# Kernel optimization log

Hardware: AMD Instinct MI355X
Metric: run time of the kernel (lower is better)

The kernel has to match this reference:

```python
import jax, jax.numpy as jnp
import numpy as np

N = 16384      # instances (cells) per bag
IN = 2000      # input_dim (genes)
E1, E2 = 1024, 512   # encoder_dims
HID = 512      # hidden_dim
NH, HD = 8, 64 # num_heads, head_dim
LK = 256       # linformer_k
EPROJ_N = 10000  # fixed in-dim of E/F projections
NEXP, MH = 4, 256  # moe experts, moe hidden (= classifier_dims[0])
C1, C2, NC = 256, 128, 2


def _ln(x, g, b):
    m = jnp.mean(x, axis=-1, keepdims=True)
    v = jnp.var(x, axis=-1, keepdims=True)
    return (x - m) * jax.lax.rsqrt(v + 1e-5) * g + b


def setup_inputs() -> dict:
    key = jax.random.key(0)
    ks = jax.random.split(key, 24)
    s = 0.02
    f32 = jnp.float32
    inp = {
        'x': jax.random.normal(ks[0], (N, IN), dtype=f32),
        'enc_w1': jax.random.normal(ks[1], (IN, E1), dtype=f32) * s,
        'enc_b1': jnp.zeros((E1,), f32),
        'enc_w2': jax.random.normal(ks[2], (E1, E2), dtype=f32) * s,
        'enc_b2': jnp.zeros((E2,), f32),
        'enc_w3': jax.random.normal(ks[3], (E2, HID), dtype=f32) * s,
        'enc_b3': jnp.zeros((HID,), f32),
        'q_w': jax.random.normal(ks[4], (HID, HID), dtype=f32) * s,
        'q_b': jnp.zeros((HID,), f32),
        'k_w': jax.random.normal(ks[5], (HID, HID), dtype=f32) * s,
        'k_b': jnp.zeros((HID,), f32),
        'v_w': jax.random.normal(ks[6], (HID, HID), dtype=f32) * s,
        'v_b': jnp.zeros((HID,), f32),
        'o_w': jax.random.normal(ks[7], (HID, HID), dtype=f32) * s,
        'o_b': jnp.zeros((HID,), f32),
        'E_w': jax.random.normal(ks[8], (LK, EPROJ_N), dtype=f32) * s,  # nn.Linear(10000, k).weight
        'F_w': jax.random.normal(ks[9], (LK, EPROJ_N), dtype=f32) * s,
        'ln1_g': jnp.ones((HID,), f32), 'ln1_b': jnp.zeros((HID,), f32),
        'ln2_g': jnp.ones((HID,), f32), 'ln2_b': jnp.zeros((HID,), f32),
        'gate_w': jax.random.normal(ks[10], (HID, NEXP), dtype=f32) * s,
        'gate_b': jnp.zeros((NEXP,), f32),
        'moe_w1': jax.random.normal(ks[11], (NEXP, HID, MH), dtype=f32) * s,
        'moe_b1': jnp.zeros((NEXP, MH), f32),
        'moe_w2': jax.random.normal(ks[12], (NEXP, MH), dtype=f32) * s,
        'moe_b2': jnp.zeros((NEXP,), f32),
        'cls_w1': jax.random.normal(ks[13], (HID, C1), dtype=f32) * s,
        'cls_b1': jnp.zeros((C1,), f32),
        'cls_w2': jax.random.normal(ks[14], (C1, C2), dtype=f32) * s,
        'cls_b2': jnp.zeros((C2,), f32),
        'cls_w3': jax.random.normal(ks[15], (C2, NC), dtype=f32) * s,
        'cls_b3': jnp.zeros((NC,), f32),
    }
    return inp


def reference(x, enc_w1, enc_b1, enc_w2, enc_b2, enc_w3, enc_b3,
              q_w, q_b, k_w, k_b, v_w, v_b, o_w, o_b, E_w, F_w,
              ln1_g, ln1_b, ln2_g, ln2_b,
              gate_w, gate_b, moe_w1, moe_b1, moe_w2, moe_b2,
              cls_w1, cls_b1, cls_w2, cls_b2, cls_w3, cls_b3):
    # --- instance encoder (chunking in torch is math-equivalent to one pass) ---
    h = jax.nn.relu(x @ enc_w1 + enc_b1)
    h = jax.nn.relu(h @ enc_w2 + enc_b2)
    feat = jax.nn.relu(h @ enc_w3 + enc_b3)          # [N, HID]
    # dropouts / InstanceDropout are identity at inference

    # --- linformer attention (single bag, batch of 1) ---
    Q = (feat @ q_w + q_b).reshape(N, NH, HD).transpose(1, 0, 2)  # [H, N, D]
    K = (feat @ k_w + k_b).reshape(N, NH, HD).transpose(1, 0, 2)
    V = (feat @ v_w + v_b).reshape(N, NH, HD).transpose(1, 0, 2)
    # N > linformer_k and the torch inner check (seq_len <= weight.size(0)=LK)
    # is false, so E/F are bilinearly resized from [10000, LK] to [LK, N], then
    # transposed to [N, LK] (matches F.interpolate align_corners=False).
    E_m = jax.image.resize(E_w.T, (LK, N), method='bilinear').T   # [N, LK]
    F_m = jax.image.resize(F_w.T, (LK, N), method='bilinear').T   # [N, LK]
    Kc = jnp.einsum('hnd,nk->hkd', K, E_m)           # [H, LK, D]
    Vc = jnp.einsum('hnd,nk->hkd', V, F_m)           # [H, LK, D]
    scores = jax.nn.softmax(jnp.einsum('hnd,hkd->hnk', Q, Kc) * (HD ** -0.5), axis=-1)
    ao = jnp.einsum('hnk,hkd->hnd', scores, Vc)      # [H, N, D]
    attn_out = ao.transpose(1, 0, 2).reshape(N, HID) @ o_w + o_b

    att = _ln(attn_out + feat, ln1_g, ln1_b)
    att = _ln(att, ln2_g, ln2_b)                     # [N, HID]

    # --- MoE MIL aggregation: gated mixture of per-expert attention pooling ---
    gates = jax.nn.softmax(jnp.mean(att, axis=0) @ gate_w + gate_b)       # [E]
    Hm = jnp.tanh(jnp.einsum('nd,edh->enh', att, moe_w1) + moe_b1[:, None, :])
    sc = jnp.einsum('enh,eh->en', Hm, moe_w2) + moe_b2[:, None]           # [E, N]
    a = jax.nn.softmax(sc, axis=1)                   # per-expert instance attention
    attn_weights = gates @ a                         # [N]
    bag = attn_weights @ att                         # [HID]

    # --- classifier ---
    c = jax.nn.relu(bag @ cls_w1 + cls_b1)
    c = jax.nn.relu(c @ cls_w2 + cls_b2)
    disease = c @ cls_w3 + cls_b3                    # [NC]
    # use_domain_adaptation=False -> no domain output
    return (bag, disease, attn_weights)
```

## Files before the change

kernel.cpp:

```cpp
#include <hip/hip_runtime.h>

#define DI __device__ __forceinline__

DI float bf2f(unsigned short u){ unsigned int v = ((unsigned int)u)<<16; float f; __builtin_memcpy(&f,&v,4); return f; }
DI unsigned short f2bf(float f){ unsigned int v; __builtin_memcpy(&v,&f,4); v = v + 0x7FFFu + ((v>>16)&1u); return (unsigned short)(v>>16); }

typedef __attribute__((ext_vector_type(8))) short bf16x8;
typedef __attribute__((ext_vector_type(4))) short short4v;
typedef __attribute__((ext_vector_type(4))) float f32x4;

#define GLD_LDS16(src, dst) __builtin_amdgcn_global_load_lds( \
    (const __attribute__((address_space(1))) void*)(src), \
    (__attribute__((address_space(3))) void*)(dst), 16, 0, 0)

DI void barrier_() { asm volatile("" ::: "memory"); __builtin_amdgcn_s_barrier(); asm volatile("" ::: "memory"); }

template<int ACT>
__global__ __launch_bounds__(256,2) void gemm5_k(
    const unsigned short* __restrict__ A, const unsigned short* __restrict__ Bt,
    const float* __restrict__ bias, unsigned short* __restrict__ C,
    int K, int lda, int ldb, int ldc)
{
  __shared__ unsigned short As[2][8192];
  __shared__ unsigned short Bs[2][8192];
  const int tid = threadIdx.x, lane = tid & 63, wid = tid >> 6;
  const int wm = wid >> 1, wn = wid & 1;
  const int q = lane >> 4, r15 = lane & 15;
  const int nx = gridDim.x;
  const int bid = blockIdx.x + nx*blockIdx.y;
  const int cpx = (nx*gridDim.y) >> 3;
  const int wg = (bid & 7)*cpx + (bid >> 3);
  const long long mBase = (long long)(wg / nx) << 7;
  const long long nBase = (long long)(wg % nx) << 7;

  f32x4 acc[4][4];
#pragma unroll
  for (int i=0;i<4;i++)
#pragma unroll
    for (int j=0;j<4;j++)
#pragma unroll
      for (int r=0;r<4;r++) acc[i][j][r] = 0.f;

  const int NT = K >> 6;

#define G5_STA(j, nb, kk) { const int d_ = tid + ((j)<<8); const int row_ = d_>>3, c_ = d_&7, sc_ = c_ ^ (row_&7); \
    GLD_LDS16(A + (mBase+row_)*(long long)lda + (kk) + (sc_<<3), &As[nb][d_<<3]); }
#define G5_STB(j, nb, kk) { const int d_ = tid + ((j)<<8); const int row_ = d_>>3, c_ = d_&7, sc_ = c_ ^ (row_&7); \
    GLD_LDS16(Bt + (nBase+row_)*(long long)ldb + (kk) + (sc_<<3), &Bs[nb][d_<<3]); }

  G5_STB(0,0,0); G5_STB(2,0,0); G5_STB(1,0,0); G5_STB(3,0,0);
  G5_STA(0,0,0); G5_STA(2,0,0); G5_STA(1,0,0); G5_STA(3,0,0);

  for (int t=0; t<NT; ++t) {
    const int b = t & 1, nb = b ^ 1;
    const bool more = (t+1 < NT);
    const int k1 = (t+1) << 6;
    bf16x8 aL[4], aH[4], bL[4], bH[4];

    asm volatile("s_waitcnt vmcnt(2)" ::: "memory");
    barrier_();
#pragma unroll
    for (int mi=0; mi<2; ++mi)
#pragma unroll
      for (int ks=0; ks<2; ++ks) {
        const int row = (wm<<6) + (mi<<4) + r15;
        const int ch = ((ks<<2)+q) ^ (row&7);
        aL[mi*2+ks] = *(const bf16x8*)&As[b][(row<<6) + (ch<<3)];
      }
#pragma unroll
    for (int ni=0; ni<2; ++ni)
#pragma unroll
      for (int ks=0; ks<2; ++ks) {
        const int col = (wn<<6) + (ni<<4) + r15;
        const int ch = ((ks<<2)+q) ^ (col&7);
        bL[ni*2+ks] = *(const bf16x8*)&Bs[b][(col<<6) + (ch<<3)];
      }
    if (more) { G5_STB(0,nb,k1); G5_STB(2,nb,k1); }
    __builtin_amdgcn_s_setprio(1);
#pragma unroll
    for (int mi=0; mi<2; ++mi)
#pragma unroll
      for (int ni=0; ni<2; ++ni)
#pragma unroll
        for (int ks=0; ks<2; ++ks)
          acc[mi][ni] = __builtin_amdgcn_mfma_f32_16x16x32_bf16(aL[mi*2+ks], bL[ni*2+ks], acc[mi][ni], 0,0,0);
    __builtin_amdgcn_s_setprio(0);
    barrier_();

#pragma unroll
    for (int ni=0; ni<2; ++ni)
#pragma unroll
      for (int ks=0; ks<2; ++ks) {
        const int col = (wn<<6) + ((ni+2)<<4) + r15;
        const int ch = ((ks<<2)+q) ^ (col&7);
        bH[ni*2+ks] = *(const bf16x8*)&Bs[b][(col<<6) + (ch<<3)];
      }
    if (more) { G5_STB(1,nb,k1); G5_STB(3,nb,k1); }
    __builtin_amdgcn_s_setprio(1);
#pragma unroll
    for (int mi=0; mi<2; ++mi)
#pragma unroll
      for (int ni=0; ni<2; ++ni)
#pragma unroll
        for (int ks=0; ks<2; ++ks)
          acc[mi][ni+2] = __builtin_amdgcn_mfma_f32_16x16x32_bf16(aL[mi*2+ks], bH[ni*2+ks], acc[mi][ni+2], 0,0,0);
    __builtin_amdgcn_s_setprio(0);

    if (more) { asm volatile("s_waitcnt vmcnt(4)" ::: "memory"); }
    else      { asm volatile("s_waitcnt vmcnt(0)" ::: "memory"); }
    barrier_();
#pragma unroll
    for (int mi=0; mi<2; ++mi)
#pragma unroll
      for (int ks=0; ks<2; ++ks) {
        const int row = (wm<<6) + ((mi+2)<<4) + r15;
        const int ch = ((ks<<2)+q) ^ (row&7);
        aH[mi*2+ks] = *(const bf16x8*)&As[b][(row<<6) + (ch<<3)];
      }
    if (more) { G5_STA(0,nb,k1); G5_STA(2,nb,k1); }
    __builtin_amdgcn_s_setprio(1);
#pragma unroll
    for (int mi=0; mi<2; ++mi)
#pragma unroll
      for (int ni=0; ni<2; ++ni)
#pragma unroll
        for (int ks=0; ks<2; ++ks)
          acc[mi+2][ni] = __builtin_amdgcn_mfma_f32_16x16x32_bf16(aH[mi*2+ks], bL[ni*2+ks], acc[mi+2][ni], 0,0,0);
    __builtin_amdgcn_s_setprio(0);
    barrier_();

    if (more) { G5_STA(1,nb,k1); G5_STA(3,nb,k1); }
    __builtin_amdgcn_s_setprio(1);
#pragma unroll
    for (int mi=0; mi<2; ++mi)
#pragma unroll
      for (int ni=0; ni<2; ++ni)
#pragma unroll
        for (int ks=0; ks<2; ++ks)
          acc[mi+2][ni+2] = __builtin_amdgcn_mfma_f32_16x16x32_bf16(aH[mi*2+ks], bH[ni*2+ks], acc[mi+2][ni+2], 0,0,0);
    __builtin_amdgcn_s_setprio(0);
  }
#undef G5_STA
#undef G5_STB

#pragma unroll
  for (int ni=0; ni<4; ++ni) {
    const long long n = nBase + (wn<<6) + (ni<<4) + r15;
    const float bval = bias[n];
#pragma unroll
    for (int mi=0; mi<4; ++mi) {
#pragma unroll
      for (int r=0; r<4; ++r) {
        const long long m = mBase + (wm<<6) + (mi<<4) + (q<<2) + r;
        float v = acc[mi][ni][r] + bval;
        if constexpr (ACT==1) v = fmaxf(v, 0.f);
        C[m*(long long)ldc + n] = f2bf(v);
      }
    }
  }
}

template<int ACT, bool MOE>
__global__ __launch_bounds__(512,2) void gemm4_k(
    const unsigned short* __restrict__ A, const unsigned short* __restrict__ Bt,
    const float* __restrict__ bias, unsigned short* __restrict__ C,
    const float* __restrict__ w2, float* __restrict__ scp,
    int K, int lda, int ldb, int ldc)
{
  __shared__ unsigned short As[2][16384];
  __shared__ unsigned short Bs[2][16384];
  const int tid = threadIdx.x, lane = tid & 63, wid = tid >> 6;
  const int wm = wid >> 2, wn = wid & 3;
  const int q = lane >> 4, r15 = lane & 15;
  const int nx = gridDim.x;
  const int bid = blockIdx.x + nx*blockIdx.y;
  const int cpx = (nx*gridDim.y) >> 3;
  const int wg = (bid & 7)*cpx + (bid >> 3);
  const long long mBase = (long long)(wg / nx) << 8;
  const long long nBase = (long long)(wg % nx) << 8;

  f32x4 acc[8][4];
#pragma unroll
  for (int i=0;i<8;i++)
#pragma unroll
    for (int j=0;j<4;j++)
#pragma unroll
      for (int r=0;r<4;r++) acc[i][j][r] = 0.f;

  const int NT = K >> 6;

#define G4_STA(j, nb, kk) { const int d_ = tid + ((j)<<9); const int row_ = d_>>3, c_ = d_&7, sc_ = c_ ^ (row_&7); \
    GLD_LDS16(A + (mBase+row_)*(long long)lda + (kk) + (sc_<<3), &As[nb][d_<<3]); }
#define G4_STB(j, nb, kk) { const int d_ = tid + ((j)<<9); const int row_ = d_>>3, c_ = d_&7, sc_ = c_ ^ (row_&7); \
    GLD_LDS16(Bt + (nBase+row_)*(long long)ldb + (kk) + (sc_<<3), &Bs[nb][d_<<3]); }

  G4_STB(0,0,0); G4_STB(1,0,0); G4_STB(2,0,0); G4_STB(3,0,0);
  G4_STA(0,0,0); G4_STA(2,0,0); G4_STA(1,0,0); G4_STA(3,0,0);

  for (int t=0; t<NT; ++t) {
    const int b = t & 1, nb = b ^ 1;
    const bool more = (t+1 < NT);
    const int k1 = (t+1) << 6;
    bf16x8 aF[8], bL[4], bH[4];

    asm volatile("s_waitcnt vmcnt(2)" ::: "memory");
    barrier_();
#pragma unroll
    for (int mi=0; mi<4; ++mi)
#pragma unroll
      for (int ks=0; ks<2; ++ks) {
        const int row = (wm<<7) + (mi<<4) + r15;
        const int ch = ((ks<<2)+q) ^ (row&7);
        aF[mi*2+ks] = *(const bf16x8*)&As[b][(row<<6) + (ch<<3)];
      }
#pragma unroll
    for (int ni=0; ni<2; ++ni)
#pragma unroll
      for (int ks=0; ks<2; ++ks) {
        const int col = (wn<<6) + (ni<<4) + r15;
        const int ch = ((ks<<2)+q) ^ (col&7);
        bL[ni*2+ks] = *(const bf16x8*)&Bs[b][(col<<6) + (ch<<3)];
      }
    if (more) { G4_STB(0,nb,k1); G4_STB(1,nb,k1); }
    __builtin_amdgcn_s_setprio(1);
#pragma unroll
    for (int mi=0; mi<4; ++mi)
#pragma unroll
      for (int ni=0; ni<2; ++ni)
#pragma unroll
        for (int ks=0; ks<2; ++ks)
          acc[mi][ni] = __builtin_amdgcn_mfma_f32_16x16x32_bf16(aF[mi*2+ks], bL[ni*2+ks], acc[mi][ni], 0,0,0);
    __builtin_amdgcn_s_setprio(0);
    barrier_();

#pragma unroll
    for (int ni=0; ni<2; ++ni)
#pragma unroll
      for (int ks=0; ks<2; ++ks) {
        const int col = (wn<<6) + ((ni+2)<<4) + r15;
        const int ch = ((ks<<2)+q) ^ (col&7);
        bH[ni*2+ks] = *(const bf16x8*)&Bs[b][(col<<6) + (ch<<3)];
      }
    if (more) { G4_STB(2,nb,k1); G4_STB(3,nb,k1); }
    __builtin_amdgcn_s_setprio(1);
#pragma unroll
    for (int mi=0; mi<4; ++mi)
#pragma unroll
      for (int ni=0; ni<2; ++ni)
#pragma unroll
        for (int ks=0; ks<2; ++ks)
          acc[mi][ni+2] = __builtin_amdgcn_mfma_f32_16x16x32_bf16(aF[mi*2+ks], bH[ni*2+ks], acc[mi][ni+2], 0,0,0);
    __builtin_amdgcn_s_setprio(0);

    if (more) { asm volatile("s_waitcnt vmcnt(4)" ::: "memory"); }
    else      { asm volatile("s_waitcnt vmcnt(0)" ::: "memory"); }
    barrier_();
#pragma unroll
    for (int mi=0; mi<4; ++mi)
#pragma unroll
      for (int ks=0; ks<2; ++ks) {
        const int row = (wm<<7) + ((mi+4)<<4) + r15;
        const int ch = ((ks<<2)+q) ^ (row&7);
        aF[mi*2+ks] = *(const bf16x8*)&As[b][(row<<6) + (ch<<3)];
      }
    if (more) { G4_STA(0,nb,k1); G4_STA(2,nb,k1); }
    __builtin_amdgcn_s_setprio(1);
#pragma unroll
    for (int mi=0; mi<4; ++mi)
#pragma unroll
      for (int ni=0; ni<2; ++ni)
#pragma unroll
        for (int ks=0; ks<2; ++ks)
          acc[mi+4][ni] = __builtin_amdgcn_mfma_f32_16x16x32_bf16(aF[mi*2+ks], bL[ni*2+ks], acc[mi+4][ni], 0,0,0);
    __builtin_amdgcn_s_setprio(0);
    barrier_();

    if (more) { G4_STA(1,nb,k1); G4_STA(3,nb,k1); }
    __builtin_amdgcn_s_setprio(1);
#pragma unroll
    for (int mi=0; mi<4; ++mi)
#pragma unroll
      for (int ni=0; ni<2; ++ni)
#pragma unroll
        for (int ks=0; ks<2; ++ks)
          acc[mi+4][ni+2] = __builtin_amdgcn_mfma_f32_16x16x32_bf16(aF[mi*2+ks], bH[ni*2+ks], acc[mi+4][ni+2], 0,0,0);
    __builtin_amdgcn_s_setprio(0);
  }
#undef G4_STA
#undef G4_STB

  if constexpr (MOE) {
    const int e = (int)(nBase >> 8);
#pragma unroll
    for (int mi=0; mi<8; ++mi) {
#pragma unroll
      for (int r=0; r<4; ++r) {
        float p = 0.f;
#pragma unroll
        for (int ni=0; ni<4; ++ni) {
          const int n = (int)nBase + (wn<<6) + (ni<<4) + r15;
          const float v = acc[mi][ni][r] + bias[n];
          const float th = 1.f - 2.f/(__expf(2.f*v) + 1.f);
          p += th * w2[n];
        }
        p += __shfl_xor(p,1,64); p += __shfl_xor(p,2,64);
        p += __shfl_xor(p,4,64); p += __shfl_xor(p,8,64);
        if (r15 == 0) {
          const long long m = mBase + (wm<<7) + (mi<<4) + (q<<2) + r;
          atomicAdd(scp + ((long long)e<<14) + m, p);
        }
      }
    }
  } else {
#pragma unroll
    for (int ni=0; ni<4; ++ni) {
      const long long n = nBase + (wn<<6) + (ni<<4) + r15;
      const float bval = bias[n];
#pragma unroll
      for (int mi=0; mi<8; ++mi) {
#pragma unroll
        for (int r=0; r<4; ++r) {
          const long long m = mBase + (wm<<7) + (mi<<4) + (q<<2) + r;
          float v = acc[mi][ni][r] + bval;
          if constexpr (ACT==1) v = fmaxf(v, 0.f);
          C[m*(long long)ldc + n] = f2bf(v);
        }
      }
    }
  }
}

DI void transpose64(const float* __restrict__ src, unsigned short* __restrict__ dst,
                    int K, int N, int Kpad, int k0, int n0, float (*tile)[65], int tid)
{
  const int c = tid & 63, rg = tid >> 6;
#pragma unroll
  for (int j=0;j<16;j++){
    const int r = (j<<2) + rg;
    const int k = k0 + r;
    tile[r][c] = (k < K) ? src[(long long)k*N + n0 + c] : 0.f;
  }
  __syncthreads();
#pragma unroll
  for (int j=0;j<16;j++){
    const int nn = (j<<2) + rg;
    dst[(long long)(n0+nn)*Kpad + k0 + c] = f2bf(tile[c][nn]);
  }
}

__global__ __launch_bounds__(256) void prep_k(
    const float* __restrict__ x, unsigned short* __restrict__ xb,
    const float* __restrict__ enc_w1, unsigned short* __restrict__ w1t,
    const float* __restrict__ enc_w2, unsigned short* __restrict__ w2t,
    const float* __restrict__ enc_w3, const float* __restrict__ q_w,
    const float* __restrict__ k_w, const float* __restrict__ v_w, const float* __restrict__ o_w,
    unsigned short* __restrict__ w3t, unsigned short* __restrict__ qkvw, unsigned short* __restrict__ owt,
    const float* __restrict__ moe_w1, unsigned short* __restrict__ mwt,
    const float* __restrict__ Ew, const float* __restrict__ Fw, float* __restrict__ t1,
    const float* __restrict__ qb, const float* __restrict__ kb, const float* __restrict__ vb,
    float* __restrict__ qkvb)
{
  __shared__ float tile[64][65];
  const int b = blockIdx.x, tid = threadIdx.x;
  if (b < 512) {
    const int k = b & 255, which = b >> 8, c = tid;
    const float* Wr = (which ? Fw : Ew) + (long long)c*10000;
    const float ksc = 39.0625f, inv = 1.f/39.0625f;
    const float sf = (k + 0.5f)*ksc - 0.5f;
    int ilo = (int)ceilf(sf - ksc); if (ilo < 0) ilo = 0;
    int ihi = (int)floorf(sf + ksc); if (ihi > 9999) ihi = 9999;
    float acc = 0.f, wsum = 0.f;
    int i = ilo;
    for (; i + 8 <= ihi + 1; i += 8) {
      float v[8];
#pragma unroll
      for (int j=0;j<8;j++) v[j] = Wr[i+j];
#pragma unroll
      for (int j=0;j<8;j++){
        const float w = fmaxf(1.f - fabsf(sf - (float)(i+j))*inv, 0.f);
        acc += w*v[j]; wsum += w;
      }
    }
    for (; i <= ihi; ++i) {
      const float w = fmaxf(1.f - fabsf(sf - (float)i)*inv, 0.f);
      acc += w * Wr[i]; wsum += w;
    }
    t1[(which*256 + k)*256 + c] = acc / wsum;
  } else if (b < 1024) {
    const int bb = b - 512;
    transpose64(enc_w1, w1t, 2000, 1024, 2048, (bb&31)<<6, (bb>>5)<<6, tile, tid);
  } else if (b < 1152) {
    const int bb = b - 1024;
    transpose64(enc_w2, w2t, 1024, 512, 1024, (bb&15)<<6, (bb>>4)<<6, tile, tid);
  } else if (b < 1472) {
    const int bb = b - 1152;
    const int z = bb >> 6, r = bb & 63;
    const float* s = (z==0)?enc_w3:(z==1)?q_w:(z==2)?k_w:(z==3)?v_w:o_w;
    unsigned short* d = (z==0)?w3t:(z==1)?qkvw:(z==2)?(qkvw+512*512):(z==3)?(qkvw+1024*512):owt;
    transpose64(s, d, 512, 512, 512, (r&7)<<6, (r>>3)<<6, tile, tid);
  } else if (b < 1600) {
    const int bb = b - 1472;
    const int z = bb >> 5, r = bb & 31;
    transpose64(moe_w1 + (long long)z*512*256, mwt + (long long)z*256*512,
                512, 256, 512, (r&7)<<6, (r>>3)<<6, tile, tid);
  } else if (b == 1600) {
#pragma unroll
    for (int i=0;i<6;i++){
      const int idx = i*256 + tid;
      const int wq = idx >> 9, off = idx & 511;
      const float* src = (wq==0)?qb:(wq==1)?kb:vb;
      qkvb[idx] = src[off];
    }
  } else if (b < 1985) {
    const int p = (b - 1601)*256 + tid;
    const int row = p / 6, cc = p - row*6;
    bf16x8 z8;
#pragma unroll
    for (int j=0;j<8;j++) z8[j]=0;
    *(bf16x8*)(xb + (long long)row*2048 + 2000 + cc*8) = z8;
  } else {
    const int bb = b - 1985;
    const long long base = (long long)bb*256 + tid;
#pragma unroll
    for (int j=0;j<16;j++){
      const long long id = base + (long long)j*524288;
      if (id < 8192000) {
        const float4 f = *((const float4*)x + id);
        const long long row = id / 500;
        const int col = (int)(id - row*500);
        short4v o;
        o[0]=(short)f2bf(f.x); o[1]=(short)f2bf(f.y); o[2]=(short)f2bf(f.z); o[3]=(short)f2bf(f.w);
        *(short4v*)(xb + row*2048 + (long long)col*4) = o;
      }
    }
  }
}

__global__ __launch_bounds__(512) void red_k(const unsigned short* __restrict__ qkv,
                                             float* __restrict__ red)
{
  const int c = blockIdx.x, which = blockIdx.y, j = threadIdx.x;
  const unsigned short* X = qkv + (which ? 1024 : 512);
  int nlo = 64*c - 32; if (nlo < 0) nlo = 0;
  int nhi = 64*c + 95; if (nhi > 16383) nhi = 16383;
  float acc = 0.f;
  for (int n=nlo; n<=nhi; ++n) {
    float sf = (n + 0.5f)*0.015625f - 0.5f;
    sf = fminf(fmaxf(sf, 0.f), 255.f);
    const int c0 = (int)sf;
    const float f = sf - (float)c0;
    float w = 0.f;
    if (c == c0) w = 1.f - f;
    else if (c == c0+1) w = f;
    if (w != 0.f) acc += w * bf2f(X[(long long)n*1536 + j]);
  }
  red[(which*256 + c)*512 + j] = acc;
}

__global__ __launch_bounds__(512) void kc_k(const float* __restrict__ t1, const float* __restrict__ red,
                                            unsigned short* __restrict__ Kc, unsigned short* __restrict__ Vct)
{
  const int k = blockIdx.x, which = blockIdx.y, j = threadIdx.x;
  const float* T = t1 + (which*256 + k)*256;
  const float* R = red + which*131072;
  float acc = 0.f;
  for (int c=0; c<256; ++c) acc += T[c] * R[c*512 + j];
  const int h = j >> 6, d = j & 63;
  if (which == 0) Kc [(h<<14) + (k<<6) + d] = f2bf(acc);
  else            Vct[(h<<14) + (d<<8) + k] = f2bf(acc);
}

__global__ __launch_bounds__(256) void attn_k(
    const unsigned short* __restrict__ Qg, const unsigned short* __restrict__ Kc,
    const unsigned short* __restrict__ Vct, unsigned short* __restrict__ ao)
{
  __shared__ unsigned short Ks[16384];
  __shared__ unsigned short Vs[16384];
  __shared__ unsigned short Ps[32768];
  const int h = blockIdx.y;
  const long long mBase = (long long)blockIdx.x << 7;
  const int tid = threadIdx.x, lane = tid & 63, wid = tid >> 6;
  const int q = lane >> 4, r15 = lane & 15;

#pragma unroll
  for (int it=0; it<8; ++it) {
    const int dbase = (it<<8) + (wid<<6);
    const int d = dbase + lane;
    {
      const int row = d >> 3, cc = d & 7, sc = cc ^ (row & 7);
      GLD_LDS16(Kc + (h<<14) + (row<<6) + (sc<<3), Ks + (dbase<<3));
    }
    {
      const int row = d >> 5, cc = d & 31, sc = (cc & 24) | ((cc ^ (row & 7)) & 7);
      GLD_LDS16(Vct + (h<<14) + (row<<8) + (sc<<3), Vs + (dbase<<3));
    }
  }
  __syncthreads();

  f32x4 acc[2][16];
#pragma unroll
  for (int mi=0;mi<2;mi++)
#pragma unroll
    for (int ni=0;ni<16;ni++)
#pragma unroll
      for (int r=0;r<4;r++) acc[mi][ni][r] = 0.f;

#pragma unroll
  for (int ks=0; ks<2; ++ks) {
    bf16x8 af[2];
#pragma unroll
    for (int mi=0; mi<2; ++mi) {
      const long long m = mBase + (wid<<5) + (mi<<4) + r15;
      af[mi] = *(const bf16x8*)(Qg + m*1536 + (h<<6) + (ks<<5) + (q<<3));
    }
#pragma unroll
    for (int ni=0; ni<16; ++ni) {
      const int col = (ni<<4) + r15;
      const int ch = ((ks<<2)+q) ^ (col&7);
      const bf16x8 bv = *(const bf16x8*)(Ks + (col<<6) + (ch<<3));
      acc[0][ni] = __builtin_amdgcn_mfma_f32_16x16x32_bf16(af[0], bv, acc[0][ni], 0,0,0);
      acc[1][ni] = __builtin_amdgcn_mfma_f32_16x16x32_bf16(af[1], bv, acc[1][ni], 0,0,0);
    }
  }

#pragma unroll
  for (int mi=0; mi<2; ++mi) {
#pragma unroll
    for (int r=0; r<4; ++r) {
      float mx = -3.4e38f;
#pragma unroll
      for (int ni=0; ni<16; ++ni) mx = fmaxf(mx, acc[mi][ni][r]);
      mx = fmaxf(mx, __shfl_xor(mx,1,64)); mx = fmaxf(mx, __shfl_xor(mx,2,64));
      mx = fmaxf(mx, __shfl_xor(mx,4,64)); mx = fmaxf(mx, __shfl_xor(mx,8,64));
      float s = 0.f;
#pragma unroll
      for (int ni=0; ni<16; ++ni) {
        const float e = __expf((acc[mi][ni][r] - mx)*0.125f);
        acc[mi][ni][r] = e; s += e;
      }
      s += __shfl_xor(s,1,64); s += __shfl_xor(s,2,64);
      s += __shfl_xor(s,4,64); s += __shfl_xor(s,8,64);
      const float inv = 1.f / s;
      const int row = (wid<<5) + (mi<<4) + (q<<2) + r;
#pragma unroll
      for (int ni=0; ni<16; ++ni) {
        const int col = (ni<<4) + r15;
        const int ch = col >> 3;
        const int chs = (ch & 24) | ((ch ^ (row & 7)) & 7);
        Ps[(row<<8) + (chs<<3) + (col&7)] = f2bf(acc[mi][ni][r]*inv);
      }
    }
  }
  __syncthreads();

  f32x4 o[2][4];
#pragma unroll
  for (int mi=0;mi<2;mi++)
#pragma unroll
    for (int ni=0;ni<4;ni++)
#pragma unroll
      for (int r=0;r<4;r++) o[mi][ni][r] = 0.f;

#pragma unroll
  for (int kk=0; kk<8; ++kk) {
    bf16x8 pa[2];
#pragma unroll
    for (int mi=0; mi<2; ++mi) {
      const int row = (wid<<5) + (mi<<4) + r15;
      const int ch = (kk<<2) + q;
      const int chs = (ch & 24) | ((ch ^ (row & 7)) & 7);
      pa[mi] = *(const bf16x8*)(Ps + (row<<8) + (chs<<3));
    }
#pragma unroll
    for (int ni=0; ni<4; ++ni) {
      const int vrow = (ni<<4) + r15;
      const int ch = (kk<<2) + q;
      const int chs = (ch & 24) | ((ch ^ (vrow & 7)) & 7);
      const bf16x8 bv = *(const bf16x8*)(Vs + (vrow<<8) + (chs<<3));
      o[0][ni] = __builtin_amdgcn_mfma_f32_16x16x32_bf16(pa[0], bv, o[0][ni], 0,0,0);
      o[1][ni] = __builtin_amdgcn_mfma_f32_16x16x32_bf16(pa[1], bv, o[1][ni], 0,0,0);
    }
  }
#pragma unroll
  for (int mi=0; mi<2; ++mi)
#pragma unroll
    for (int ni=0; ni<4; ++ni)
#pragma unroll
      for (int r=0; r<4; ++r) {
        const long long m = mBase + (wid<<5) + (mi<<4) + (q<<2) + r;
        ao[m*512 + (h<<6) + (ni<<4) + r15] = f2bf(o[mi][ni][r]);
      }
}

__global__ __launch_bounds__(256) void ln64_k(
    const unsigned short* __restrict__ attno, const unsigned short* __restrict__ feat,
    const float* __restrict__ g1, const float* __restrict__ b1,
    const float* __restrict__ g2, const float* __restrict__ b2,
    unsigned short* __restrict__ att, float* __restrict__ colp, float* __restrict__ scp)
{
  __shared__ float cred[4][512];
  const int tid = threadIdx.x, lane = tid & 63, wid = tid >> 6;
  const int c0 = lane << 3;
  scp[((long long)blockIdx.x<<8) + tid] = 0.f;
  float g1v[8], b1v[8], g2v[8], b2v[8];
#pragma unroll
  for (int j=0;j<8;j++){ g1v[j]=g1[c0+j]; b1v[j]=b1[c0+j]; g2v[j]=g2[c0+j]; b2v[j]=b2[c0+j]; }
  float cacc[8];
#pragma unroll
  for (int j=0;j<8;j++) cacc[j]=0.f;
  for (int rr=0; rr<16; ++rr) {
    const long long row = ((long long)blockIdx.x<<6) + (rr<<2) + wid;
    const bf16x8 a = *(const bf16x8*)(attno + (row<<9) + c0);
    const bf16x8 f = *(const bf16x8*)(feat  + (row<<9) + c0);
    float xv[8]; float s=0.f, qs=0.f;
#pragma unroll
    for (int j=0;j<8;j++){ xv[j] = bf2f((unsigned short)a[j]) + bf2f((unsigned short)f[j]); s += xv[j]; qs += xv[j]*xv[j]; }
#pragma unroll
    for (int o=32;o;o>>=1){ s += __shfl_xor(s,o,64); qs += __shfl_xor(qs,o,64); }
    float m = s*(1.f/512.f);
    float rs = rsqrtf(qs*(1.f/512.f) - m*m + 1e-5f);
    float y[8]; s=0.f; qs=0.f;
#pragma unroll
    for (int j=0;j<8;j++){ y[j] = (xv[j]-m)*rs*g1v[j] + b1v[j]; s += y[j]; qs += y[j]*y[j]; }
#pragma unroll
    for (int o=32;o;o>>=1){ s += __shfl_xor(s,o,64); qs += __shfl_xor(qs,o,64); }
    m = s*(1.f/512.f);
    rs = rsqrtf(qs*(1.f/512.f) - m*m + 1e-5f);
    bf16x8 ov;
#pragma unroll
    for (int j=0;j<8;j++){ const float z = (y[j]-m)*rs*g2v[j] + b2v[j]; cacc[j] += z; ov[j] = (short)f2bf(z); }
    *(bf16x8*)(att + (row<<9) + c0) = ov;
  }
#pragma unroll
  for (int j=0;j<8;j++) cred[wid][c0+j] = cacc[j];
  __syncthreads();
  {
    const float v0 = cred[0][tid]+cred[1][tid]+cred[2][tid]+cred[3][tid];
    const float v1 = cred[0][tid+256]+cred[1][tid+256]+cred[2][tid+256]+cred[3][tid+256];
    colp[((long long)blockIdx.x<<9)+tid]     = v0;
    colp[((long long)blockIdx.x<<9)+tid+256] = v1;
  }
}

__global__ __launch_bounds__(512) void meangates_k(const float* __restrict__ part,
    const float* __restrict__ gw, const float* __restrict__ gb, float* __restrict__ gates)
{
  __shared__ float mv[512];
  __shared__ float tmp[4];
  const int t = threadIdx.x;
  float s = 0.f;
  for (int b=0;b<256;b++) s += part[(b<<9)+t];
  mv[t] = s * (1.f/16384.f);
  __syncthreads();
  if (t < 4) {
    float a = gb[t];
    for (int d=0; d<512; ++d) a += mv[d]*gw[d*4+t];
    tmp[t] = a;
  }
  __syncthreads();
  if (t == 0) {
    const float m = fmaxf(fmaxf(tmp[0],tmp[1]),fmaxf(tmp[2],tmp[3]));
    float e[4]; float ss=0.f;
    for (int i=0;i<4;i++){ e[i]=__expf(tmp[i]-m); ss+=e[i]; }
    for (int i=0;i<4;i++) gates[i] = e[i]/ss;
  }
}

__global__ __launch_bounds__(1024) void moestat_k(const float* __restrict__ sc,
                                                  float* __restrict__ mstat, float* __restrict__ sstat)
{
  __shared__ float red[1024];
  const int e = blockIdx.x, t = threadIdx.x;
  const float* p = sc + e*16384;
  float m = -3.4e38f;
  for (int n=t; n<16384; n+=1024) m = fmaxf(m, p[n]);
  red[t] = m; __syncthreads();
  for (int o=512;o;o>>=1){ if (t<o) red[t]=fmaxf(red[t],red[t+o]); __syncthreads(); }
  m = red[0]; __syncthreads();
  float s = 0.f;
  for (int n=t; n<16384; n+=1024) s += __expf(p[n]-m);
  red[t] = s; __syncthreads();
  for (int o=512;o;o>>=1){ if (t<o) red[t]+=red[t+o]; __syncthreads(); }
  if (t==0){ mstat[e]=m; sstat[e]=red[0]; }
}

__global__ __launch_bounds__(256) void wbag_k(const unsigned short* __restrict__ att,
    const float* __restrict__ scp, const float* __restrict__ gates,
    const float* __restrict__ mstat, const float* __restrict__ sstat,
    float* __restrict__ part, float* __restrict__ dout)
{
  __shared__ float wrow[128];
  const int c = threadIdx.x;
  const long long r0 = (long long)blockIdx.x * 128;
  if (c < 128) {
    const long long n = r0 + c;
    float w = 0.f;
#pragma unroll
    for (int e=0;e<4;e++) w += gates[e]*__expf(scp[((long long)e<<14)+n]-mstat[e]) / sstat[e];
    wrow[c] = w;
    dout[514 + n] = w;
  }
  __syncthreads();
  float a0=0.f, a1=0.f;
  for (int r=0;r<128;r++){
    const float w = wrow[r];
    const unsigned short* p = att + ((r0+r)<<9);
    a0 += w*bf2f(p[c]); a1 += w*bf2f(p[c+256]);
  }
  part[((long long)blockIdx.x<<9)+c]     = a0;
  part[((long long)blockIdx.x<<9)+c+256] = a1;
}

__global__ __launch_bounds__(512) void cls2_k(const float* __restrict__ bagp,
    const float* __restrict__ w1, const float* __restrict__ b1,
    const float* __restrict__ w2, const float* __restrict__ b2,
    const float* __restrict__ w3, const float* __restrict__ b3, float* __restrict__ dout)
{
  __shared__ float bag[512]; __shared__ float c1[256]; __shared__ float c2[128];
  const int tid = threadIdx.x;
  float s = 0.f;
  for (int b=0;b<128;b++) s += bagp[(b<<9)+tid];
  bag[tid] = s; dout[tid] = s;
  __syncthreads();
  if (tid < 256) {
    float a = b1[tid];
    for (int d=0; d<512; ++d) a += bag[d]*w1[d*256+tid];
    c1[tid] = fmaxf(a, 0.f);
  }
  __syncthreads();
  if (tid < 128) {
    float a2 = b2[tid];
    for (int d=0; d<256; ++d) a2 += c1[d]*w2[d*128+tid];
    c2[tid] = fmaxf(a2, 0.f);
  }
  __syncthreads();
  if (tid < 2) {
    float a3 = b3[tid];
    for (int d=0; d<128; ++d) a3 += c2[d]*w3[d*2+tid];
    dout[512 + tid] = a3;
  }
}

extern "C" void kernel_launch(void* const* d_in, const int* in_sizes, int n_in,
                              void* d_out, int out_size, void* d_ws, size_t ws_size,
                              hipStream_t stream)
{
  (void)in_sizes; (void)n_in; (void)out_size; (void)ws_size;
  const float* x      = (const float*)d_in[0];
  const float* enc_w1 = (const float*)d_in[1];
  const float* enc_b1 = (const float*)d_in[2];
  const float* enc_w2 = (const float*)d_in[3];
  const float* enc_b2 = (const float*)d_in[4];
  const float* enc_w3 = (const float*)d_in[5];
  const float* enc_b3 = (const float*)d_in[6];
  const float* q_w    = (const float*)d_in[7];
  const float* q_b    = (const float*)d_in[8];
  const float* k_w    = (const float*)d_in[9];
  const float* k_b    = (const float*)d_in[10];
  const float* v_w    = (const float*)d_in[11];
  const float* v_b    = (const float*)d_in[12];
  const float* o_w    = (const float*)d_in[13];
  const float* o_b    = (const float*)d_in[14];
  const float* E_w    = (const float*)d_in[15];
  const float* F_w    = (const float*)d_in[16];
  const float* ln1_g  = (const float*)d_in[17];
  const float* ln1_b  = (const float*)d_in[18];
  const float* ln2_g  = (const float*)d_in[19];
  const float* ln2_b  = (const float*)d_in[20];
  const float* gate_w = (const float*)d_in[21];
  const float* gate_b = (const float*)d_in[22];
  const float* moe_w1 = (const float*)d_in[23];
  const float* moe_b1 = (const float*)d_in[24];
  const float* moe_w2 = (const float*)d_in[25];
  const float* cls_w1 = (const float*)d_in[27];
  const float* cls_b1 = (const float*)d_in[28];
  const float* cls_w2 = (const float*)d_in[29];
  const float* cls_b2 = (const float*)d_in[30];
  const float* cls_w3 = (const float*)d_in[31];
  const float* cls_b3 = (const float*)d_in[32];

  char* ws = (char*)d_ws;
  const size_t MB = 1024*1024;
  unsigned short* x_bf  = (unsigned short*)(ws + 0);
  unsigned short* h1    = (unsigned short*)(ws + 64*MB);
  unsigned short* h2    = (unsigned short*)(ws + 0);
  unsigned short* feat  = (unsigned short*)(ws + 16*MB);
  unsigned short* qkv   = (unsigned short*)(ws + 32*MB);
  unsigned short* ao    = (unsigned short*)(ws + 80*MB);
  unsigned short* attno = (unsigned short*)(ws + 0);
  unsigned short* att   = (unsigned short*)(ws + 96*MB);
  unsigned short* w1t   = (unsigned short*)(ws + 112*MB);
  unsigned short* w2t   = (unsigned short*)(ws + 116*MB);
  unsigned short* w3t   = (unsigned short*)(ws + 117*MB);
  unsigned short* qkvw  = (unsigned short*)(ws + 117*MB + 512*1024);
  unsigned short* owt   = (unsigned short*)(ws + 119*MB);
  unsigned short* mwt   = (unsigned short*)(ws + 119*MB + 512*1024);
  float*  t1b   = (float*)(ws + 120*MB + 512*1024);
  float*  redb  = (float*)(ws + 121*MB);
  unsigned short* Kcbf  = (unsigned short*)(ws + 122*MB);
  unsigned short* Vctbf = (unsigned short*)(ws + 122*MB + 256*1024);
  float*  colp  = (float*)(ws + 122*MB + 512*1024);
  float*  bagp  = (float*)(ws + 123*MB);
  float*  qkvb  = (float*)(ws + 123*MB + 256*1024);
  float*  gatesp= (float*)(ws + 123*MB + 264*1024);
  float*  scp   = (float*)(ws + 123*MB + 268*1024);
  float*  mstat = (float*)(ws + 123*MB + 524*1024);
  float*  sstat = (float*)(ws + 123*MB + 524*1024 + 64);
  float*  dout  = (float*)d_out;

  prep_k<<<4033,256,0,stream>>>(x, x_bf, enc_w1, w1t, enc_w2, w2t,
                                enc_w3, q_w, k_w, v_w, o_w, w3t, qkvw, owt,
                                moe_w1, mwt, E_w, F_w, t1b, q_b, k_b, v_b, qkvb);

  gemm4_k<1,false><<<dim3(4,64,1),512,0,stream>>>(x_bf, w1t, enc_b1, h1, nullptr,nullptr, 2048,2048,2048,1024);
  gemm5_k<1><<<dim3(4,128,1),256,0,stream>>>(h1, w2t, enc_b2, h2,   1024,1024,1024, 512);
  gemm5_k<1><<<dim3(4,128,1),256,0,stream>>>(h2, w3t, enc_b3, feat,  512, 512, 512, 512);
  gemm5_k<0><<<dim3(12,128,1),256,0,stream>>>(feat, qkvw, qkvb, qkv, 512,512,512,1536);
  red_k<<<dim3(256,2),512,0,stream>>>(qkv, redb);
  kc_k <<<dim3(256,2),512,0,stream>>>(t1b, redb, Kcbf, Vctbf);
  attn_k<<<dim3(128,8),256,0,stream>>>(qkv, Kcbf, Vctbf, ao);
  gemm5_k<0><<<dim3(4,128,1),256,0,stream>>>(ao, owt, o_b, attno, 512,512,512,512);
  ln64_k<<<256,256,0,stream>>>(attno, feat, ln1_g, ln1_b, ln2_g, ln2_b, att, colp, scp);
  meangates_k<<<1,512,0,stream>>>(colp, gate_w, gate_b, gatesp);
  gemm4_k<0,true><<<dim3(4,64,1),512,0,stream>>>(att, mwt, moe_b1, nullptr, moe_w2, scp, 512,512,512,0);
  moestat_k<<<4,1024,0,stream>>>(scp, mstat, sstat);
  wbag_k<<<128,256,0,stream>>>(att, scp, gatesp, mstat, sstat, bagp, dout);
  cls2_k<<<1,512,0,stream>>>(bagp, cls_w1, cls_b1, cls_w2, cls_b2, cls_w3, cls_b3, dout);
}
```

Before: 431.8 us.

## Fuse fp32-to-bf16 input conversion into first encoder GEMM

Drops the separate pass that converts x to a padded bf16 copy in prep_k. A new GEMM kernel reads x directly as fp32 and converts to bf16 in registers before writing swizzled tiles to LDS, while B still uses direct global-to-LDS loads. This removes a full write and re-read of the converted 16384x2048 activation, at the cost of twice the global read bytes for A inside the GEMM and register-staged A loads with conversion work in the main loop.

```diff
diff --git a/kernel.cpp b/kernel.cpp
--- a/kernel.cpp
+++ b/kernel.cpp
@@ -6,7 +6,6 @@
 DI unsigned short f2bf(float f){ unsigned int v; __builtin_memcpy(&v,&f,4); v = v + 0x7FFFu + ((v>>16)&1u); return (unsigned short)(v>>16); }
 
 typedef __attribute__((ext_vector_type(8))) short bf16x8;
-typedef __attribute__((ext_vector_type(4))) short short4v;
 typedef __attribute__((ext_vector_type(4))) float f32x4;
 
 #define GLD_LDS16(src, dst) __builtin_amdgcn_global_load_lds( \
@@ -14,6 +13,142 @@
     (__attribute__((address_space(3))) void*)(dst), 16, 0, 0)
 
 DI void barrier_() { asm volatile("" ::: "memory"); __builtin_amdgcn_s_barrier(); asm volatile("" ::: "memory"); }
+
+template<int ACT>
+__global__ __launch_bounds__(512) void gemm6_k(
+    const float* __restrict__ A, const unsigned short* __restrict__ Bt,
+    const float* __restrict__ bias, unsigned short* __restrict__ C,
+    int lda, int ldb, int ldc)
+{
+  __shared__ unsigned short As[2][16384];
+  __shared__ unsigned short Bs[2][16384];
+  const int tid = threadIdx.x, lane = tid & 63, wid = tid >> 6;
+  const int wm = wid >> 2, wn = wid & 3;
+  const int q = lane >> 4, r15 = lane & 15;
+  const int nx = gridDim.x;
+  const int bid = blockIdx.x + nx*blockIdx.y;
+  const int cpx = (nx*gridDim.y) >> 3;
+  const int wg = (bid & 7)*cpx + (bid >> 3);
+  const long long mBase = (long long)(wg / nx) << 8;
+  const long long nBase = (long long)(wg % nx) << 8;
+
+  f32x4 acc[8][4];
+#pragma unroll
+  for (int i=0;i<8;i++)
+#pragma unroll
+    for (int j=0;j<4;j++)
+#pragma unroll
+      for (int r=0;r<4;r++) acc[i][j][r] = 0.f;
+
+  const int NT = 32;
+  float4 aL[8];
+
+#define G6_LDA(kk) { _Pragma("unroll") for (int j=0;j<4;j++){ \
+    const int d_ = tid + (j<<9); const int row_ = d_>>3, cc_ = d_&7; \
+    const int col8 = (kk) + (cc_<<3); \
+    if (col8 < 2000) { \
+      const float* p_ = A + (mBase+row_)*(long long)lda + col8; \
+      aL[2*j] = *(const float4*)p_; aL[2*j+1] = *(const float4*)(p_+4); \
+    } else { aL[2*j] = make_float4(0.f,0.f,0.f,0.f); aL[2*j+1] = make_float4(0.f,0.f,0.f,0.f); } } }
+#define G6_WRA(nb) { _Pragma("unroll") for (int j=0;j<4;j++){ \
+    const int d_ = tid + (j<<9); const int row_ = d_>>3, cc_ = d_&7; const int sc_ = cc_ ^ (row_&7); \
+    bf16x8 v_; \
+    v_[0]=(short)f2bf(aL[2*j].x);   v_[1]=(short)f2bf(aL[2*j].y); \
+    v_[2]=(short)f2bf(aL[2*j].z);   v_[3]=(short)f2bf(aL[2*j].w); \
+    v_[4]=(short)f2bf(aL[2*j+1].x); v_[5]=(short)f2bf(aL[2*j+1].y); \
+    v_[6]=(short)f2bf(aL[2*j+1].z); v_[7]=(short)f2bf(aL[2*j+1].w); \
+    *(bf16x8*)&As[nb][(d_>>3<<6) + (sc_<<3)] = v_; } }
+#define G6_STB(nb, kk) { _Pragma("unroll") for (int j=0;j<4;j++){ \
+    const int d_ = tid + (j<<9); const int row_ = d_>>3, c_ = d_&7, sc_ = c_ ^ (row_&7); \
+    GLD_LDS16(Bt + (nBase+row_)*(long long)ldb + (kk) + (sc_<<3), &Bs[nb][d_<<3]); } }
+
+  G6_LDA(0);
+  G6_STB(0, 0);
+  asm volatile("s_waitcnt vmcnt(0)" ::: "memory");
+  G6_WRA(0);
+  __syncthreads();
+
+  for (int t=0; t<NT; ++t) {
+    const int b = t & 1, nb = b ^ 1;
+    const bool more = (t+1 < NT);
+    const int k1 = (t+1) << 6;
+    if (more) { G6_LDA(k1); G6_STB(nb, k1); }
+
+    bf16x8 aF[8], bL[4], bH[4];
+#pragma unroll
+    for (int mi=0; mi<4; ++mi)
+#pragma unroll
+      for (int ks=0; ks<2; ++ks) {
+        const int row = (wm<<7) + (mi<<4) + r15;
+        const int ch = ((ks<<2)+q) ^ (row&7);
+        aF[mi*2+ks] = *(const bf16x8*)&As[b][(row<<6) + (ch<<3)];
+      }
+#pragma unroll
+    for (int ni=0; ni<2; ++ni)
+#pragma unroll
+      for (int ks=0; ks<2; ++ks) {
+        const int colL = (wn<<6) + (ni<<4) + r15;
+        const int colH = (wn<<6) + ((ni+2)<<4) + r15;
+        bL[ni*2+ks] = *(const bf16x8*)&Bs[b][(colL<<6) + ((((ks<<2)+q) ^ (colL&7))<<3)];
+        bH[ni*2+ks] = *(const bf16x8*)&Bs[b][(colH<<6) + ((((ks<<2)+q) ^ (colH&7))<<3)];
+      }
+    __builtin_amdgcn_s_setprio(1);
+#pragma unroll
+    for (int mi=0; mi<4; ++mi)
+#pragma unroll
+      for (int ni=0; ni<2; ++ni)
+#pragma unroll
+        for (int ks=0; ks<2; ++ks) {
+          acc[mi][ni]   = __builtin_amdgcn_mfma_f32_16x16x32_bf16(aF[mi*2+ks], bL[ni*2+ks], acc[mi][ni],   0,0,0);
+          acc[mi][ni+2] = __builtin_amdgcn_mfma_f32_16x16x32_bf16(aF[mi*2+ks], bH[ni*2+ks], acc[mi][ni+2], 0,0,0);
+        }
+    __builtin_amdgcn_s_setprio(0);
+#pragma unroll
+    for (int mi=0; mi<4; ++mi)
+#pragma unroll
+      for (int ks=0; ks<2; ++ks) {
+        const int row = (wm<<7) + ((mi+4)<<4) + r15;
+        const int ch = ((ks<<2)+q) ^ (row&7);
+        aF[mi*2+ks] = *(const bf16x8*)&As[b][(row<<6) + (ch<<3)];
+      }
+    __builtin_amdgcn_s_setprio(1);
+#pragma unroll
+    for (int mi=0; mi<4; ++mi)
+#pragma unroll
+      for (int ni=0; ni<2; ++ni)
+#pragma unroll
+        for (int ks=0; ks<2; ++ks) {
+          acc[mi+4][ni]   = __builtin_amdgcn_mfma_f32_16x16x32_bf16(aF[mi*2+ks], bL[ni*2+ks], acc[mi+4][ni],   0,0,0);
+          acc[mi+4][ni+2] = __builtin_amdgcn_mfma_f32_16x16x32_bf16(aF[mi*2+ks], bH[ni*2+ks], acc[mi+4][ni+2], 0,0,0);
+        }
+    __builtin_amdgcn_s_setprio(0);
+
+    if (more) {
+      asm volatile("s_waitcnt vmcnt(0)" ::: "memory");
+      G6_WRA(nb);
+    }
+    __syncthreads();
+  }
+#undef G6_LDA
+#undef G6_WRA
+#undef G6_STB
+
+#pragma unroll
+  for (int ni=0; ni<4; ++ni) {
+    const long long n = nBase + (wn<<6) + (ni<<4) + r15;
+    const float bval = bias[n];
+#pragma unroll
+    for (int mi=0; mi<8; ++mi) {
+#pragma unroll
+      for (int r=0; r<4; ++r) {
+        const long long m = mBase + (wm<<7) + (mi<<4) + (q<<2) + r;
+        float v = acc[mi][ni][r] + bval;
+        if constexpr (ACT==1) v = fmaxf(v, 0.f);
+        C[m*(long long)ldc + n] = f2bf(v);
+      }
+    }
+  }
+}
 
 template<int ACT>
 __global__ __launch_bounds__(256,2) void gemm5_k(
@@ -349,7 +484,6 @@
 }
 
 __global__ __launch_bounds__(256) void prep_k(
-    const float* __restrict__ x, unsigned short* __restrict__ xb,
     const float* __restrict__ enc_w1, unsigned short* __restrict__ w1t,
     const float* __restrict__ enc_w2, unsigned short* __restrict__ w2t,
     const float* __restrict__ enc_w3, const float* __restrict__ q_w,
@@ -403,35 +537,13 @@
     const int z = bb >> 5, r = bb & 31;
     transpose64(moe_w1 + (long long)z*512*256, mwt + (long long)z*256*512,
                 512, 256, 512, (r&7)<<6, (r>>3)<<6, tile, tid);
-  } else if (b == 1600) {
+  } else {
 #pragma unroll
     for (int i=0;i<6;i++){
       const int idx = i*256 + tid;
       const int wq = idx >> 9, off = idx & 511;
       const float* src = (wq==0)?qb:(wq==1)?kb:vb;
       qkvb[idx] = src[off];
-    }
-  } else if (b < 1985) {
-    const int p = (b - 1601)*256 + tid;
-    const int row = p / 6, cc = p - row*6;
-    bf16x8 z8;
-#pragma unroll
-    for (int j=0;j<8;j++) z8[j]=0;
-    *(bf16x8*)(xb + (long long)row*2048 + 2000 + cc*8) = z8;
-  } else {
-    const int bb = b - 1985;
-    const long long base = (long long)bb*256 + tid;
-#pragma unroll
-    for (int j=0;j<16;j++){
-      const long long id = base + (long long)j*524288;
-      if (id < 8192000) {
-        const float4 f = *((const float4*)x + id);
-        const long long row = id / 500;
-        const int col = (int)(id - row*500);
-        short4v o;
-        o[0]=(short)f2bf(f.x); o[1]=(short)f2bf(f.y); o[2]=(short)f2bf(f.z); o[3]=(short)f2bf(f.w);
-        *(short4v*)(xb + row*2048 + (long long)col*4) = o;
-      }
     }
   }
 }
@@ -781,7 +893,6 @@
 
   char* ws = (char*)d_ws;
   const size_t MB = 1024*1024;
-  unsigned short* x_bf  = (unsigned short*)(ws + 0);
   unsigned short* h1    = (unsigned short*)(ws + 64*MB);
   unsigned short* h2    = (unsigned short*)(ws + 0);
   unsigned short* feat  = (unsigned short*)(ws + 16*MB);
@@ -808,11 +919,11 @@
   float*  sstat = (float*)(ws + 123*MB + 524*1024 + 64);
   float*  dout  = (float*)d_out;
 
-  prep_k<<<4033,256,0,stream>>>(x, x_bf, enc_w1, w1t, enc_w2, w2t,
+  prep_k<<<1601,256,0,stream>>>(enc_w1, w1t, enc_w2, w2t,
                                 enc_w3, q_w, k_w, v_w, o_w, w3t, qkvw, owt,
                                 moe_w1, mwt, E_w, F_w, t1b, q_b, k_b, v_b, qkvb);
 
-  gemm4_k<1,false><<<dim3(4,64,1),512,0,stream>>>(x_bf, w1t, enc_b1, h1, nullptr,nullptr, 2048,2048,2048,1024);
+  gemm6_k<1><<<dim3(4,64,1),512,0,stream>>>(x, w1t, enc_b1, h1, 2000,2048,1024);
   gemm5_k<1><<<dim3(4,128,1),256,0,stream>>>(h1, w2t, enc_b2, h2,   1024,1024,1024, 512);
   gemm5_k<1><<<dim3(4,128,1),256,0,stream>>>(h2, w3t, enc_b3, feat,  512, 512, 512, 512);
   gemm5_k<0><<<dim3(12,128,1),256,0,stream>>>(feat, qkvw, qkvb, qkv, 512,512,512,1536);
```

After: 483.3 us. 11.9% more time.
